# Kernel tuning notes

Measured on AMD Instinct MI355X. Metric: run time of the kernel, lower is better.

Reference implementation:

```python
import jax, jax.numpy as jnp
import numpy as np

KSIZE = 3
RES_SCALE = 0.2
WITH_RESIDUAL = True


def setup_inputs() -> dict:
    key = jax.random.key(0)
    x = jax.random.normal(key, (8, 3, 1024, 1024), dtype=jnp.float32)
    return {"x": x}


def reference(x) -> jnp.ndarray:
    B, C, H, W = x.shape
    k = KSIZE
    p = k // 2
    # zero padding matches F.unfold(padding=k//2)
    xp = jnp.pad(x, ((0, 0), (0, 0), (p, p), (p, p)))
    # [B, C, k*k, H, W] stack of shifted views (k*k = 9, small static loop)
    patches = jnp.stack(
        [xp[:, :, di:di + H, dj:dj + W] for di in range(k) for dj in range(k)],
        axis=2,
    )
    # median of odd-sized window = middle element of sorted values
    med = jnp.sort(patches, axis=2)[:, :, (k * k) // 2]
    if WITH_RESIDUAL:
        return x + RES_SCALE * (med - x)
    return med
```

## Files before the change

kernel.cpp:

```cpp
#include <hip/hip_runtime.h>


typedef float v4f __attribute__((ext_vector_type(4)));

#define S2(a,b) { float _t=fminf(a,b); (b)=fmaxf(a,b); (a)=_t; }

__device__ __forceinline__ float med3f(float a, float b, float c) {
    return fmaxf(fminf(a, b), fminf(fmaxf(a, b), c));
}
__device__ __forceinline__ float max3f(float a, float b, float c) {
    return fmaxf(a, fmaxf(b, c));
}
__device__ __forceinline__ float min3f(float a, float b, float c) {
    return fminf(a, fminf(b, c));
}

constexpr int W  = 1024, H = 1024;
constexpr int RS = 16;
constexpr int P  = 6;

__global__ __launch_bounds__(256, 6) void median_blur_kernel(
    const float* __restrict__ xin, float* __restrict__ out)
{
    const int tx = threadIdx.x;
    const int x0 = tx << 2;
    const int y0 = (int)blockIdx.x * RS;
    const size_t plane = (size_t)blockIdx.y * (size_t)(H * W);
    const float* base  = xin + plane;
    float*       obase = out + plane;

    const bool lE = (tx == 0);
    const bool rE = (tx == 255);
    const int  xl = lE ? x0       : x0 - 1;
    const int  xr = rE ? x0 + 3   : x0 + 4;

    v4f   cc[P];
    float ll[P], rr[P];

    const v4f vz = {0.0f, 0.0f, 0.0f, 0.0f};

#pragma unroll
    for (int s = 0; s < P - 1; ++s) {
        const int y = y0 - 1 + s;
        if (s == 0 && y < 0) {
            cc[s] = vz; ll[s] = 0.0f; rr[s] = 0.0f;
        } else {
            const float* rp = base + ((size_t)y << 10);
            cc[s] = *reinterpret_cast<const v4f*>(rp + x0);
            ll[s] = rp[xl];
            rr[s] = rp[xr];
        }
    }

#pragma unroll
    for (int i = 0; i < RS; ++i) {
        if (i + P - 1 <= RS + 1) {
            const int s    = i + P - 1;
            const int slot = s % P;
            const int y    = y0 - 1 + s;
            if (s == RS + 1 && y >= H) {
                cc[slot] = vz; ll[slot] = 0.0f; rr[slot] = 0.0f;
            } else {
                const float* rp = base + ((size_t)y << 10);
                cc[slot] = *reinterpret_cast<const v4f*>(rp + x0);
                ll[slot] = rp[xl];
                rr[slot] = rp[xr];
            }
            __builtin_amdgcn_sched_barrier(0);
        }

        const int sT = i % P, sM = (i + 1) % P, sB = (i + 2) % P;

        const float t0 = lE ? 0.0f : ll[sT], t5 = rE ? 0.0f : rr[sT];
        const float m0 = lE ? 0.0f : ll[sM], m5 = rE ? 0.0f : rr[sM];
        const float b0 = lE ? 0.0f : ll[sB], b5 = rE ? 0.0f : rr[sB];
        const float t[6] = { t0, cc[sT].x, cc[sT].y, cc[sT].z, cc[sT].w, t5 };
        const float m[6] = { m0, cc[sM].x, cc[sM].y, cc[sM].z, cc[sM].w, m5 };
        const float b[6] = { b0, cc[sB].x, cc[sB].y, cc[sB].z, cc[sB].w, b5 };

        float lo[6], mi[6], hi[6];
#pragma unroll
        for (int j = 0; j < 6; ++j) {
            float a = t[j], c0 = m[j], d = b[j];
            S2(a, c0); S2(c0, d); S2(a, c0);
            lo[j] = a; mi[j] = c0; hi[j] = d;
        }
        v4f o;
#pragma unroll
        for (int j = 0; j < 4; ++j) {
            const float mxlo = max3f(lo[j], lo[j + 1], lo[j + 2]);
            const float mnhi = min3f(hi[j], hi[j + 1], hi[j + 2]);
            const float mdmi = med3f(mi[j], mi[j + 1], mi[j + 2]);
            const float med  = med3f(mxlo, mdmi, mnhi);
            const float xc   = m[j + 1];
            o[j] = xc + 0.2f * (med - xc);
        }
        __builtin_nontemporal_store(o,
            reinterpret_cast<v4f*>(obase + ((size_t)(y0 + i) << 10) + x0));
    }
}

extern "C" void kernel_launch(void* const* d_in, const int* in_sizes, int n_in,
                              void* d_out, int out_size, void* d_ws, size_t ws_size,
                              hipStream_t stream) {
    const float* x = (const float*)d_in[0];
    float* out = (float*)d_out;
    const int planes = in_sizes[0] / (H * W);
    dim3 block(256);
    dim3 grid(H / RS, planes);
    median_blur_kernel<<<grid, block, 0, stream>>>(x, out);
}
```

Baseline: 174.9 us.

## Stage input rows through an LDS ring with async global-to-LDS loads

Input rows are no longer loaded straight into registers. They are copied into a 6-slot shared-memory ring with global_load_lds DMA and hand-tuned vmcnt waits plus barriers, and each thread reads its 4-wide centre and halo pixels from LDS. This removes the two redundant scalar halo global loads per row and lets the DMA run ahead of compute. In exchange it adds a block barrier per row, uses 24KB of LDS per block, which may limit occupancy, and switches the output from nontemporal to regular stores.

```diff
diff --git a/kernel.cpp b/kernel.cpp
--- a/kernel.cpp
+++ b/kernel.cpp
@@ -4,24 +4,25 @@
 typedef float v4f __attribute__((ext_vector_type(4)));
 
 #define S2(a,b) { float _t=fminf(a,b); (b)=fmaxf(a,b); (a)=_t; }
-
 __device__ __forceinline__ float med3f(float a, float b, float c) {
     return fmaxf(fminf(a, b), fminf(fmaxf(a, b), c));
-}
-__device__ __forceinline__ float max3f(float a, float b, float c) {
-    return fmaxf(a, fmaxf(b, c));
-}
-__device__ __forceinline__ float min3f(float a, float b, float c) {
-    return fminf(a, fminf(b, c));
 }
 
 constexpr int W  = 1024, H = 1024;
 constexpr int RS = 16;
-constexpr int P  = 6;
+constexpr int NS = 6;
+
+typedef const __attribute__((address_space(1))) void gld_g;
+typedef __attribute__((address_space(3))) void gld_s;
+
+#define WAITV(n)  asm volatile("s_waitcnt vmcnt(" #n ")" ::: "memory")
+#define BARRIER() asm volatile("s_barrier" ::: "memory")
 
 __global__ __launch_bounds__(256, 6) void median_blur_kernel(
     const float* __restrict__ xin, float* __restrict__ out)
 {
+    __shared__ float ring[NS][W];
+
     const int tx = threadIdx.x;
     const int x0 = tx << 2;
     const int y0 = (int)blockIdx.x * RS;
@@ -29,54 +30,63 @@
     const float* base  = xin + plane;
     float*       obase = out + plane;
 
-    const bool lE = (tx == 0);
-    const bool rE = (tx == 255);
-    const int  xl = lE ? x0       : x0 - 1;
-    const int  xr = rE ? x0 + 3   : x0 + 4;
+    const bool lE = (tx == 0), rE = (tx == 255);
+    const int  xl = lE ? 0     : x0 - 1;
+    const int  xr = rE ? W - 1 : x0 + 4;
+    const bool topB = (blockIdx.x == 0);
+    const bool botB = (blockIdx.x == (H / RS) - 1);
 
-    v4f   cc[P];
-    float ll[P], rr[P];
+    float win[3][6];
 
-    const v4f vz = {0.0f, 0.0f, 0.0f, 0.0f};
+    auto DMA = [&](int k) {
+        int y = y0 - 1 + k;
+        y = y < 0 ? 0 : (y > H - 1 ? H - 1 : y);
+        const float* g = base + ((size_t)y << 10) + x0;
+        __builtin_amdgcn_global_load_lds((gld_g*)g, (gld_s*)&ring[k % NS][x0], 16, 0, 0);
+    };
+    auto RD = [&](int k) {
+        const int s = k % NS;
+        v4f c = *reinterpret_cast<const v4f*>(&ring[s][x0]);
+        float hl = ring[s][xl];
+        float hr = ring[s][xr];
+        float* w = win[k % 3];
+        w[0] = lE ? 0.0f : hl;
+        w[1] = c.x; w[2] = c.y; w[3] = c.z; w[4] = c.w;
+        w[5] = rE ? 0.0f : hr;
+    };
 
 #pragma unroll
-    for (int s = 0; s < P - 1; ++s) {
-        const int y = y0 - 1 + s;
-        if (s == 0 && y < 0) {
-            cc[s] = vz; ll[s] = 0.0f; rr[s] = 0.0f;
-        } else {
-            const float* rp = base + ((size_t)y << 10);
-            cc[s] = *reinterpret_cast<const v4f*>(rp + x0);
-            ll[s] = rp[xl];
-            rr[s] = rp[xr];
-        }
+    for (int k = 0; k < 5; ++k) DMA(k);
+    WAITV(3);
+    BARRIER();
+    RD(0); RD(1);
+    if (topB) {
+#pragma unroll
+        for (int j = 0; j < 6; ++j) win[0][j] = 0.0f;
     }
 
 #pragma unroll
     for (int i = 0; i < RS; ++i) {
-        if (i + P - 1 <= RS + 1) {
-            const int s    = i + P - 1;
-            const int slot = s % P;
-            const int y    = y0 - 1 + s;
-            if (s == RS + 1 && y >= H) {
-                cc[slot] = vz; ll[slot] = 0.0f; rr[slot] = 0.0f;
-            } else {
-                const float* rp = base + ((size_t)y << 10);
-                cc[slot] = *reinterpret_cast<const v4f*>(rp + x0);
-                ll[slot] = rp[xl];
-                rr[slot] = rp[xr];
-            }
-            __builtin_amdgcn_sched_barrier(0);
+        if (i + 5 <= RS + 1) DMA(i + 5);
+
+        if      (i == 0)            WAITV(3);
+        else if (i == 1)            WAITV(4);
+        else if (i == 2 || i == 13) WAITV(5);
+        else if (i == 14)           WAITV(4);
+        else if (i == 15)           WAITV(3);
+        else                        WAITV(6);
+
+        BARRIER();
+
+        RD(i + 2);
+        if (i == RS - 1 && botB) {
+#pragma unroll
+            for (int j = 0; j < 6; ++j) win[(i + 2) % 3][j] = 0.0f;
         }
 
-        const int sT = i % P, sM = (i + 1) % P, sB = (i + 2) % P;
-
-        const float t0 = lE ? 0.0f : ll[sT], t5 = rE ? 0.0f : rr[sT];
-        const float m0 = lE ? 0.0f : ll[sM], m5 = rE ? 0.0f : rr[sM];
-        const float b0 = lE ? 0.0f : ll[sB], b5 = rE ? 0.0f : rr[sB];
-        const float t[6] = { t0, cc[sT].x, cc[sT].y, cc[sT].z, cc[sT].w, t5 };
-        const float m[6] = { m0, cc[sM].x, cc[sM].y, cc[sM].z, cc[sM].w, m5 };
-        const float b[6] = { b0, cc[sB].x, cc[sB].y, cc[sB].z, cc[sB].w, b5 };
+        const float* t = win[i % 3];
+        const float* m = win[(i + 1) % 3];
+        const float* b = win[(i + 2) % 3];
 
         float lo[6], mi[6], hi[6];
 #pragma unroll
@@ -88,15 +98,14 @@
         v4f o;
 #pragma unroll
         for (int j = 0; j < 4; ++j) {
-            const float mxlo = max3f(lo[j], lo[j + 1], lo[j + 2]);
-            const float mnhi = min3f(hi[j], hi[j + 1], hi[j + 2]);
+            const float mxlo = fmaxf(lo[j], fmaxf(lo[j + 1], lo[j + 2]));
+            const float mnhi = fminf(hi[j], fminf(hi[j + 1], hi[j + 2]));
             const float mdmi = med3f(mi[j], mi[j + 1], mi[j + 2]);
             const float med  = med3f(mxlo, mdmi, mnhi);
             const float xc   = m[j + 1];
             o[j] = xc + 0.2f * (med - xc);
         }
-        __builtin_nontemporal_store(o,
-            reinterpret_cast<v4f*>(obase + ((size_t)(y0 + i) << 10) + x0));
+        *reinterpret_cast<v4f*>(obase + ((size_t)(y0 + i) << 10) + x0) = o;
     }
 }
 
```

Measured after the change: 178.0 us. About the same (+1.8%).
